# Performance work log

Hardware: AMD Instinct MI355X
Metric: run time of the kernel (lower is better)

Reference implementation:

```python
import jax, jax.numpy as jnp
import numpy as np

N_NODES = 100000
N_EDGES = 1600000
IN_FEATS = 256
DIMS = [IN_FEATS, 128, 64, 16, 40]


def setup_inputs() -> dict:
    key = jax.random.key(0)
    ks = jax.random.split(key, 3 + 2 * 4)
    x = jax.random.normal(ks[0], (N_NODES, IN_FEATS), dtype=jnp.float32)
    src = jax.random.randint(ks[1], (N_EDGES,), 0, N_NODES)
    dst = jax.random.randint(ks[2], (N_EDGES,), 0, N_NODES)
    inp = {"x": x, "src": src, "dst": dst}
    for i in range(4):
        fan_in = DIMS[i]
        inp[f"W{i+1}"] = jax.random.normal(ks[3 + 2 * i], (DIMS[i], DIMS[i + 1]), dtype=jnp.float32) / np.sqrt(fan_in)
        inp[f"b{i+1}"] = jnp.zeros((DIMS[i + 1],), dtype=jnp.float32)
    return inp


def reference(x, src, dst, W1, b1, W2, b2, W3, b3, W4, b4):
    n = x.shape[0]
    ones = jnp.ones(src.shape[0], dtype=x.dtype)
    # symmetric GCN normalization (DGL norm='both'); clamp deg>=1 like DGL
    deg_out = jnp.maximum(jax.ops.segment_sum(ones, src, num_segments=n), 1.0)
    deg_in = jnp.maximum(jax.ops.segment_sum(ones, dst, num_segments=n), 1.0)
    norm_src = jax.lax.rsqrt(deg_out)[:, None]  # [N,1]
    norm_dst = jax.lax.rsqrt(deg_in)[:, None]   # [N,1]

    def gconv(h, W, b, act):
        # project first (in_feats >= out_feats for every layer, matching DGL ordering)
        h = (h * norm_src) @ W                                   # [N, d_out]
        h = jax.ops.segment_sum(h[src], dst, num_segments=n)      # SpMM aggregate
        h = h * norm_dst + b
        return jax.nn.relu(h) if act else h

    h = gconv(x, W1, b1, True)
    h = gconv(h, W2, b2, True)
    h = gconv(h, W3, b3, True)
    h = gconv(h, W4, b4, False)
    return h
```

## Files before the change

kernel.cpp:

```cpp
#include <hip/hip_runtime.h>


typedef unsigned short ushort_t;
#define CAP 64

__device__ __forceinline__ void gload_lds16(const float4* g, float4* l) {
    __builtin_amdgcn_global_load_lds(
        (const __attribute__((address_space(1))) void*)g,
        (__attribute__((address_space(3))) void*)l, 16, 0, 0);
}

__device__ __forceinline__ ushort_t f2bf(float f) {
    unsigned u = __float_as_uint(f);
    u += 0x7FFFu + ((u >> 16) & 1u);
    return (ushort_t)(u >> 16);
}
__device__ __forceinline__ unsigned pack2bf(float a, float b) {
    return (unsigned)f2bf(a) | ((unsigned)f2bf(b) << 16);
}
#define BFLO(u) __uint_as_float((u) << 16)
#define BFHI(u) __uint_as_float((u) & 0xffff0000u)

template<int DIN, int DOUT, int RB, int KT, typename EPI>
__device__ __forceinline__ void proj_body(
        const float* __restrict__ in, const float* __restrict__ W,
        int N, int n0, float4* __restrict__ wlds, float4* __restrict__ xlds,
        EPI&& epi) {
    constexpr int CG  = DOUT / 4;
    constexpr int RPP = 256 / CG;
    constexpr int R4  = RB / RPP;
    constexpr int K4T = KT / 4;
    constexpr int NKT = DIN / KT;
    constexpr int XTILE = RB * K4T;
    constexpr int WTILE = KT * CG;
    static_assert(RPP * CG == 256, "full block");
    static_assert((K4T & (K4T - 1)) == 0, "pow2 swizzle");
    static_assert(XTILE % 256 == 0 && WTILE % 256 == 0, "stage granularity");

    const int tid  = threadIdx.x;
    const int wave = tid >> 6;
    const int lane = tid & 63;
    const int rp   = tid / CG;
    const int cg   = tid - rp * CG;

    float4 acc[R4];
#pragma unroll
    for (int r = 0; r < R4; ++r) acc[r] = make_float4(0.f, 0.f, 0.f, 0.f);

    for (int kt = 0; kt < NKT; ++kt) {
        const float4* wsrc = (const float4*)(W + (size_t)kt * KT * DOUT);
#pragma unroll
        for (int j = 0; j < WTILE / 256; ++j) {
            int base = j * 256 + wave * 64;
            gload_lds16(wsrc + base + lane, &wlds[base]);
        }
#pragma unroll
        for (int j = 0; j < XTILE / 256; ++j) {
            int base = j * 256 + wave * 64;
            int fi   = base + lane;
            int row  = fi / K4T;
            int k4   = fi - row * K4T;
            int k4s  = k4 ^ (row & (K4T - 1));
            int grow = n0 + row; if (grow >= N) grow = N - 1;
            const float4* gsrc = (const float4*)(in + (size_t)grow * DIN) + kt * K4T + k4s;
            gload_lds16(gsrc, &xlds[base]);
        }
        __syncthreads();
#pragma unroll 2
        for (int k4 = 0; k4 < K4T; ++k4) {
            float4 w0 = wlds[(k4 * 4 + 0) * CG + cg];
            float4 w1 = wlds[(k4 * 4 + 1) * CG + cg];
            float4 w2 = wlds[(k4 * 4 + 2) * CG + cg];
            float4 w3 = wlds[(k4 * 4 + 3) * CG + cg];
#pragma unroll
            for (int r = 0; r < R4; ++r) {
                int row = rp + r * RPP;
                float4 xv = xlds[row * K4T + (k4 ^ (row & (K4T - 1)))];
                acc[r].x = fmaf(xv.x, w0.x, acc[r].x);
                acc[r].y = fmaf(xv.x, w0.y, acc[r].y);
                acc[r].z = fmaf(xv.x, w0.z, acc[r].z);
                acc[r].w = fmaf(xv.x, w0.w, acc[r].w);
                acc[r].x = fmaf(xv.y, w1.x, acc[r].x);
                acc[r].y = fmaf(xv.y, w1.y, acc[r].y);
                acc[r].z = fmaf(xv.y, w1.z, acc[r].z);
                acc[r].w = fmaf(xv.y, w1.w, acc[r].w);
                acc[r].x = fmaf(xv.z, w2.x, acc[r].x);
                acc[r].y = fmaf(xv.z, w2.y, acc[r].y);
                acc[r].z = fmaf(xv.z, w2.z, acc[r].z);
                acc[r].w = fmaf(xv.z, w2.w, acc[r].w);
                acc[r].x = fmaf(xv.w, w3.x, acc[r].x);
                acc[r].y = fmaf(xv.w, w3.y, acc[r].y);
                acc[r].z = fmaf(xv.w, w3.z, acc[r].z);
                acc[r].w = fmaf(xv.w, w3.w, acc[r].w);
            }
        }
        __syncthreads();
    }
    epi(acc, rp, cg);
}

template<int DIN, int DOUT, int RB, int KT>
__global__ void __launch_bounds__(256) k_comb(
        const float* __restrict__ x, const float* __restrict__ W,
        ushort_t* __restrict__ outbf, int N,
        const int* __restrict__ src, const int* __restrict__ dst,
        int* __restrict__ degO, int* __restrict__ degI,
        int* __restrict__ colp, int E, int PB, int HTH) {
    constexpr int CG  = DOUT / 4;
    constexpr int RPP = 256 / CG;
    constexpr int R4  = RB / RPP;
    constexpr int K4T = KT / 4;
    __shared__ float4 wlds[KT * CG];
    __shared__ float4 xlds[RB * K4T];

    int bid = blockIdx.x, g = bid / 5, r = bid - g * 5;
    if (r == 4) {
        int i = g * 256 + (int)threadIdx.x;
        for (; i < E; i += HTH) {
            int s = src[i];
            int d = dst[i];
            atomicAdd(&degO[s], 1);
            int rk = atomicAdd(&degI[d], 1);
            if (rk < CAP) colp[(size_t)d * CAP + rk] = s;
        }
        return;
    }
    int pidx = g * 4 + r;
    if (pidx >= PB) return;
    int n0 = pidx * RB;
    proj_body<DIN, DOUT, RB, KT>(x, W, N, n0, wlds, xlds,
        [&](float4 (&acc)[R4], int rp, int cg) {
#pragma unroll
            for (int rr = 0; rr < R4; ++rr) {
                int n = n0 + rp + rr * RPP;
                if (n < N) {
                    ushort4 s;
                    s.x = f2bf(acc[rr].x); s.y = f2bf(acc[rr].y);
                    s.z = f2bf(acc[rr].z); s.w = f2bf(acc[rr].w);
                    *(ushort4*)(outbf + (size_t)n * DOUT + cg * 4) = s;
                }
            }
        });
}

__global__ void k_prep(const int* __restrict__ degO, const int* __restrict__ degI,
                       float* __restrict__ nSf, float* __restrict__ nDf, int N) {
    int i = blockIdx.x * 256 + threadIdx.x;
    if (i < N) {
        int a = degO[i]; nSf[i] = rsqrtf((float)(a > 1 ? a : 1));
        int b = degI[i]; nDf[i] = rsqrtf((float)(b > 1 ? b : 1));
    }
}

__global__ void __launch_bounds__(256) k_proj_l2bf(
        const ushort_t* __restrict__ in, const float* __restrict__ nrm,
        const float* __restrict__ W, ushort_t* __restrict__ outbf, int N) {
    __shared__ float4 wlds[32 * 16];
    __shared__ uint4  xlds[64 * 4];
    const int tid = threadIdx.x;
    const int rp = tid >> 4, cg = tid & 15;
    int n0 = blockIdx.x * 64;

    float4 acc[4];
#pragma unroll
    for (int r = 0; r < 4; ++r) acc[r] = make_float4(0.f, 0.f, 0.f, 0.f);

    for (int kt = 0; kt < 4; ++kt) {
        const float4* wsrc = (const float4*)(W + (size_t)kt * 32 * 64);
        gload_lds16(wsrc + tid, &wlds[tid]);
        gload_lds16(wsrc + 256 + tid, &wlds[256 + tid]);
        {
            int row = tid >> 2, c = tid & 3;
            int cs = c ^ (row & 3);
            int grow = n0 + row; if (grow >= N) grow = N - 1;
            const uint4* gsrc = (const uint4*)(in + (size_t)grow * 128) + kt * 4 + cs;
            gload_lds16((const float4*)gsrc, (float4*)&xlds[tid]);
        }
        __syncthreads();
#pragma unroll
        for (int k8 = 0; k8 < 4; ++k8) {
            float4 w[8];
#pragma unroll
            for (int j = 0; j < 8; ++j) w[j] = wlds[(k8 * 8 + j) * 16 + cg];
#pragma unroll
            for (int r = 0; r < 4; ++r) {
                int row = rp + r * 16;
                uint4 xv = xlds[row * 4 + (k8 ^ (row & 3))];
                float xf[8] = { BFLO(xv.x), BFHI(xv.x), BFLO(xv.y), BFHI(xv.y),
                                BFLO(xv.z), BFHI(xv.z), BFLO(xv.w), BFHI(xv.w) };
#pragma unroll
                for (int j = 0; j < 8; ++j) {
                    acc[r].x = fmaf(xf[j], w[j].x, acc[r].x);
                    acc[r].y = fmaf(xf[j], w[j].y, acc[r].y);
                    acc[r].z = fmaf(xf[j], w[j].z, acc[r].z);
                    acc[r].w = fmaf(xf[j], w[j].w, acc[r].w);
                }
            }
        }
        __syncthreads();
    }
#pragma unroll
    for (int r = 0; r < 4; ++r) {
        int n = n0 + rp + r * 16;
        if (n < N) {
            float nm = nrm[n];
            ushort4 s;
            s.x = f2bf(acc[r].x * nm); s.y = f2bf(acc[r].y * nm);
            s.z = f2bf(acc[r].z * nm); s.w = f2bf(acc[r].w * nm);
            *(ushort4*)(outbf + (size_t)n * 64 + cg * 4) = s;
        }
    }
}

__global__ void __launch_bounds__(256) k_gather_l1(
        const int* __restrict__ colp, const int* __restrict__ degI,
        const float* __restrict__ nSf, const float* __restrict__ nDf,
        const ushort_t* __restrict__ projbf, const float* __restrict__ bias,
        ushort_t* __restrict__ outbf, int N) {
    constexpr int DOUT = 128;
    constexpr int CGB = DOUT / 8;
    long t = blockIdx.x * 256L + threadIdx.x;
    if (t >= (long)N * CGB) return;
    int n  = (int)(t / CGB);
    int cb = (int)(t - (long)n * CGB);
    const int* cl = colp + (size_t)n * CAP;
    int dg = degI[n]; if (dg > CAP) dg = CAP;
    float acc[8];
#pragma unroll
    for (int k = 0; k < 8; ++k) acc[k] = 0.f;
    int i = 0;
    for (; i + 4 <= dg; i += 4) {
        int4 ss = *(const int4*)(cl + i);
        uint4 v0 = *(const uint4*)(projbf + (size_t)ss.x * DOUT + cb * 8);
        uint4 v1 = *(const uint4*)(projbf + (size_t)ss.y * DOUT + cb * 8);
        uint4 v2 = *(const uint4*)(projbf + (size_t)ss.z * DOUT + cb * 8);
        uint4 v3 = *(const uint4*)(projbf + (size_t)ss.w * DOUT + cb * 8);
        float n0 = nSf[ss.x], n1 = nSf[ss.y], n2 = nSf[ss.z], n3 = nSf[ss.w];
        acc[0] = fmaf(n0, BFLO(v0.x), fmaf(n1, BFLO(v1.x), fmaf(n2, BFLO(v2.x), fmaf(n3, BFLO(v3.x), acc[0]))));
        acc[1] = fmaf(n0, BFHI(v0.x), fmaf(n1, BFHI(v1.x), fmaf(n2, BFHI(v2.x), fmaf(n3, BFHI(v3.x), acc[1]))));
        acc[2] = fmaf(n0, BFLO(v0.y), fmaf(n1, BFLO(v1.y), fmaf(n2, BFLO(v2.y), fmaf(n3, BFLO(v3.y), acc[2]))));
        acc[3] = fmaf(n0, BFHI(v0.y), fmaf(n1, BFHI(v1.y), fmaf(n2, BFHI(v2.y), fmaf(n3, BFHI(v3.y), acc[3]))));
        acc[4] = fmaf(n0, BFLO(v0.z), fmaf(n1, BFLO(v1.z), fmaf(n2, BFLO(v2.z), fmaf(n3, BFLO(v3.z), acc[4]))));
        acc[5] = fmaf(n0, BFHI(v0.z), fmaf(n1, BFHI(v1.z), fmaf(n2, BFHI(v2.z), fmaf(n3, BFHI(v3.z), acc[5]))));
        acc[6] = fmaf(n0, BFLO(v0.w), fmaf(n1, BFLO(v1.w), fmaf(n2, BFLO(v2.w), fmaf(n3, BFLO(v3.w), acc[6]))));
        acc[7] = fmaf(n0, BFHI(v0.w), fmaf(n1, BFHI(v1.w), fmaf(n2, BFHI(v2.w), fmaf(n3, BFHI(v3.w), acc[7]))));
    }
    for (; i < dg; ++i) {
        int s0 = cl[i];
        uint4 v0 = *(const uint4*)(projbf + (size_t)s0 * DOUT + cb * 8);
        float ns0 = nSf[s0];
        acc[0] = fmaf(ns0, BFLO(v0.x), acc[0]);
        acc[1] = fmaf(ns0, BFHI(v0.x), acc[1]);
        acc[2] = fmaf(ns0, BFLO(v0.y), acc[2]);
        acc[3] = fmaf(ns0, BFHI(v0.y), acc[3]);
        acc[4] = fmaf(ns0, BFLO(v0.z), acc[4]);
        acc[5] = fmaf(ns0, BFHI(v0.z), acc[5]);
        acc[6] = fmaf(ns0, BFLO(v0.w), acc[6]);
        acc[7] = fmaf(ns0, BFHI(v0.w), acc[7]);
    }
    float nm = nDf[n];
    const float* bp = bias + cb * 8;
    float o[8];
#pragma unroll
    for (int k = 0; k < 8; ++k) o[k] = fmaxf(fmaf(acc[k], nm, bp[k]), 0.f);
    uint4 s;
    s.x = pack2bf(o[0], o[1]); s.y = pack2bf(o[2], o[3]);
    s.z = pack2bf(o[4], o[5]); s.w = pack2bf(o[6], o[7]);
    *(uint4*)(outbf + (size_t)n * DOUT + cb * 8) = s;
}

__global__ void __launch_bounds__(256) k_gather_fuse2(
        const int* __restrict__ colp, const int* __restrict__ degI,
        const float* __restrict__ nSf, const float* __restrict__ nDf,
        const ushort_t* __restrict__ p2bf, const float* __restrict__ b2,
        const float* __restrict__ W3, float* __restrict__ P3, int N) {
    constexpr int DOUT = 64;
    __shared__ float w3s[64 * 16];
    ((float4*)w3s)[threadIdx.x] = ((const float4*)W3)[threadIdx.x];
    __syncthreads();

    long t = blockIdx.x * 256L + threadIdx.x;
    int n = (int)(t >> 3);
    bool valid = n < N;
    if (!valid) n = N - 1;
    int cb = (int)(t & 7);
    int lane = threadIdx.x & 63;
    int gb = lane & ~7;

    const int* cl = colp + (size_t)n * CAP;
    int dg = degI[n]; if (dg > CAP) dg = CAP;
    float acc[8];
#pragma unroll
    for (int k = 0; k < 8; ++k) acc[k] = 0.f;
    int i = 0;
    for (; i + 4 <= dg; i += 4) {
        int4 ss = *(const int4*)(cl + i);
        uint4 v0 = *(const uint4*)(p2bf + (size_t)ss.x * DOUT + cb * 8);
        uint4 v1 = *(const uint4*)(p2bf + (size_t)ss.y * DOUT + cb * 8);
        uint4 v2 = *(const uint4*)(p2bf + (size_t)ss.z * DOUT + cb * 8);
        uint4 v3 = *(const uint4*)(p2bf + (size_t)ss.w * DOUT + cb * 8);
        acc[0] += BFLO(v0.x) + BFLO(v1.x) + BFLO(v2.x) + BFLO(v3.x);
        acc[1] += BFHI(v0.x) + BFHI(v1.x) + BFHI(v2.x) + BFHI(v3.x);
        acc[2] += BFLO(v0.y) + BFLO(v1.y) + BFLO(v2.y) + BFLO(v3.y);
        acc[3] += BFHI(v0.y) + BFHI(v1.y) + BFHI(v2.y) + BFHI(v3.y);
        acc[4] += BFLO(v0.z) + BFLO(v1.z) + BFLO(v2.z) + BFLO(v3.z);
        acc[5] += BFHI(v0.z) + BFHI(v1.z) + BFHI(v2.z) + BFHI(v3.z);
        acc[6] += BFLO(v0.w) + BFLO(v1.w) + BFLO(v2.w) + BFLO(v3.w);
        acc[7] += BFHI(v0.w) + BFHI(v1.w) + BFHI(v2.w) + BFHI(v3.w);
    }
    for (; i < dg; ++i) {
        int s0 = cl[i];
        uint4 v0 = *(const uint4*)(p2bf + (size_t)s0 * DOUT + cb * 8);
        acc[0] += BFLO(v0.x); acc[1] += BFHI(v0.x);
        acc[2] += BFLO(v0.y); acc[3] += BFHI(v0.y);
        acc[4] += BFLO(v0.z); acc[5] += BFHI(v0.z);
        acc[6] += BFLO(v0.w); acc[7] += BFHI(v0.w);
    }
    float nm = nDf[n];
    float ns = nSf[n];
    const float* bp = b2 + cb * 8;
    float o[8];
#pragma unroll
    for (int k = 0; k < 8; ++k)
        o[k] = fmaxf(fmaf(acc[k], nm, bp[k]), 0.f) * ns;
    float y0 = 0.f, y1 = 0.f;
#pragma unroll
    for (int k = 0; k < 64; ++k) {
        float v = __shfl(o[k & 7], gb + (k >> 3), 64);
        y0 = fmaf(v, w3s[k * 16 + 2 * cb], y0);
        y1 = fmaf(v, w3s[k * 16 + 2 * cb + 1], y1);
    }
    if (valid) *(float2*)(P3 + (size_t)n * 16 + 2 * cb) = make_float2(y0, y1);
}

__global__ void __launch_bounds__(256) k_gather_l3(
        const int* __restrict__ colp, const int* __restrict__ degI,
        const float* __restrict__ nSf, const float* __restrict__ nDf,
        const float* __restrict__ proj, const float* __restrict__ bias,
        float* __restrict__ out, int N) {
    long t = blockIdx.x * 256L + threadIdx.x;
    if (t >= (long)N * 4) return;
    int n  = (int)(t >> 2);
    int cg = (int)(t & 3);
    const int* cl = colp + (size_t)n * CAP;
    int dg = degI[n]; if (dg > CAP) dg = CAP;
    float4 a0 = make_float4(0.f, 0.f, 0.f, 0.f);
    float4 a1 = make_float4(0.f, 0.f, 0.f, 0.f);
    float4 a2 = make_float4(0.f, 0.f, 0.f, 0.f);
    float4 a3 = make_float4(0.f, 0.f, 0.f, 0.f);
    int i = 0;
    for (; i + 4 <= dg; i += 4) {
        int4 ss = *(const int4*)(cl + i);
        float4 v0 = *(const float4*)(proj + (size_t)ss.x * 16 + cg * 4);
        float4 v1 = *(const float4*)(proj + (size_t)ss.y * 16 + cg * 4);
        float4 v2 = *(const float4*)(proj + (size_t)ss.z * 16 + cg * 4);
        float4 v3 = *(const float4*)(proj + (size_t)ss.w * 16 + cg * 4);
        a0.x += v0.x; a0.y += v0.y; a0.z += v0.z; a0.w += v0.w;
        a1.x += v1.x; a1.y += v1.y; a1.z += v1.z; a1.w += v1.w;
        a2.x += v2.x; a2.y += v2.y; a2.z += v2.z; a2.w += v2.w;
        a3.x += v3.x; a3.y += v3.y; a3.z += v3.z; a3.w += v3.w;
    }
    for (; i < dg; ++i) {
        int s0 = cl[i];
        float4 v0 = *(const float4*)(proj + (size_t)s0 * 16 + cg * 4);
        a0.x += v0.x; a0.y += v0.y; a0.z += v0.z; a0.w += v0.w;
    }
    float4 s = make_float4(a0.x + a1.x + a2.x + a3.x, a0.y + a1.y + a2.y + a3.y,
                           a0.z + a1.z + a2.z + a3.z, a0.w + a1.w + a2.w + a3.w);
    float nm = nDf[n];
    float ns = nSf[n];
    float4 b = *(const float4*)(bias + cg * 4);
    float4 o;
    o.x = fmaxf(fmaf(s.x, nm, b.x), 0.f) * ns;
    o.y = fmaxf(fmaf(s.y, nm, b.y), 0.f) * ns;
    o.z = fmaxf(fmaf(s.z, nm, b.z), 0.f) * ns;
    o.w = fmaxf(fmaf(s.w, nm, b.w), 0.f) * ns;
    *(float4*)(out + (size_t)n * 16 + cg * 4) = o;
}

__global__ void __launch_bounds__(256) k_gather_fuse4(
        const int* __restrict__ colp, const int* __restrict__ degI,
        const float* __restrict__ nDf, const float* __restrict__ t4,
        const float* __restrict__ W4, const float* __restrict__ b4,
        float* __restrict__ out, int N) {
    __shared__ float w4s[16 * 40];
    __shared__ float b4s[40];
    for (int i = threadIdx.x; i < 160; i += 256)
        ((float4*)w4s)[i] = ((const float4*)W4)[i];
    if (threadIdx.x < 40) b4s[threadIdx.x] = b4[threadIdx.x];
    __syncthreads();

    long t = blockIdx.x * 256L + threadIdx.x;
    int n = (int)(t >> 2);
    bool valid = n < N;
    if (!valid) n = N - 1;
    int cg = (int)(t & 3);
    int lane = threadIdx.x & 63;
    int gb = lane & ~3;

    const int* cl = colp + (size_t)n * CAP;
    int dg = degI[n]; if (dg > CAP) dg = CAP;
    float4 a0 = make_float4(0.f, 0.f, 0.f, 0.f);
    float4 a1 = make_float4(0.f, 0.f, 0.f, 0.f);
    int i = 0;
    for (; i + 2 <= dg; i += 2) {
        int2 ss = *(const int2*)(cl + i);
        float4 v0 = *(const float4*)(t4 + (size_t)ss.x * 16 + cg * 4);
        float4 v1 = *(const float4*)(t4 + (size_t)ss.y * 16 + cg * 4);
        a0.x += v0.x; a0.y += v0.y; a0.z += v0.z; a0.w += v0.w;
        a1.x += v1.x; a1.y += v1.y; a1.z += v1.z; a1.w += v1.w;
    }
    if (i < dg) {
        int s0 = cl[i];
        float4 v0 = *(const float4*)(t4 + (size_t)s0 * 16 + cg * 4);
        a0.x += v0.x; a0.y += v0.y; a0.z += v0.z; a0.w += v0.w;
    }
    float av[4] = { a0.x + a1.x, a0.y + a1.y, a0.z + a1.z, a0.w + a1.w };

    float y[10];
#pragma unroll
    for (int jj = 0; jj < 10; ++jj) y[jj] = 0.f;
#pragma unroll
    for (int k = 0; k < 16; ++k) {
        float v = __shfl(av[k & 3], gb + (k >> 2), 64);
        const float* wr = w4s + k * 40 + cg * 10;
#pragma unroll
        for (int jj = 0; jj < 10; ++jj) y[jj] = fmaf(v, wr[jj], y[jj]);
    }
    if (valid) {
        float nm = nDf[n];
        float* dp = out + (size_t)n * 40 + cg * 10;
        const float* bp = b4s + cg * 10;
#pragma unroll
        for (int jj = 0; jj < 10; ++jj) dp[jj] = fmaf(y[jj], nm, bp[jj]);
    }
}

static inline int cdiv(long a, int b) { return (int)((a + b - 1) / b); }

extern "C" void kernel_launch(void* const* d_in, const int* in_sizes, int n_in,
                              void* d_out, int out_size, void* d_ws, size_t ws_size,
                              hipStream_t stream) {
    const float* x   = (const float*)d_in[0];
    const int*   src = (const int*)d_in[1];
    const int*   dst = (const int*)d_in[2];
    const float* W1 = (const float*)d_in[3];  const float* b1 = (const float*)d_in[4];
    const float* W2 = (const float*)d_in[5];  const float* b2 = (const float*)d_in[6];
    const float* W3 = (const float*)d_in[7];  const float* b3 = (const float*)d_in[8];
    const float* W4 = (const float*)d_in[9];  const float* b4 = (const float*)d_in[10];

    const int N = in_sizes[0] / 256;
    const int E = in_sizes[1];

    int* ws_i = (int*)d_ws;
    int* degO   = ws_i;
    int* degI   = ws_i + N;
    int* colp   = ws_i + 2 * (size_t)N;
    float* nSf  = (float*)(ws_i + 2 * (size_t)N + (size_t)N * CAP);
    float* nDf  = nSf + N;
    float* projb = nDf + N;
    float* hbuf  = projb + (size_t)N * 64;
    ushort_t* projbf = (ushort_t*)projb;
    ushort_t* h1bf   = (ushort_t*)hbuf;
    float* P3 = projb + (size_t)N * 32;

    int PB = cdiv(N, 64);
    int G5 = cdiv(PB, 4);
    int HTH = G5 * 256;

    hipMemsetAsync(degO, 0, 2 * (size_t)N * sizeof(int), stream);
    k_comb<256, 128, 64, 32><<<5 * G5, 256, 0, stream>>>(
        x, W1, projbf, N, src, dst, degO, degI, colp, E, PB, HTH);

    k_prep<<<cdiv(N, 256), 256, 0, stream>>>(degO, degI, nSf, nDf, N);

    k_gather_l1<<<cdiv((long)N * 16, 256), 256, 0, stream>>>(
        colp, degI, nSf, nDf, projbf, b1, h1bf, N);

    k_proj_l2bf<<<cdiv(N, 64), 256, 0, stream>>>(h1bf, nSf, W2, projbf, N);
    k_gather_fuse2<<<cdiv((long)N * 8, 256), 256, 0, stream>>>(
        colp, degI, nSf, nDf, projbf, b2, W3, P3, N);

    k_gather_l3<<<cdiv((long)N * 4, 256), 256, 0, stream>>>(
        colp, degI, nSf, nDf, P3, b3, hbuf, N);

    k_gather_fuse4<<<cdiv((long)N * 4, 256), 256, 0, stream>>>(
        colp, degI, nDf, hbuf, W4, b4, (float*)d_out, N);
}
```

Measured before the change: 353.8 us.

## Split CSR fill by destination half to overlap with layer-1 gather

```diff
diff --git a/kernel.cpp b/kernel.cpp
--- a/kernel.cpp
+++ b/kernel.cpp
@@ -17,6 +17,9 @@
 }
 __device__ __forceinline__ unsigned pack2bf(float a, float b) {
     return (unsigned)f2bf(a) | ((unsigned)f2bf(b) << 16);
+}
+__device__ __forceinline__ float nrm_of(int d) {
+    return rsqrtf((float)(d > 1 ? d : 1));
 }
 #define BFLO(u) __uint_as_float((u) << 16)
 #define BFHI(u) __uint_as_float((u) & 0xffff0000u)
@@ -33,9 +36,6 @@
     constexpr int NKT = DIN / KT;
     constexpr int XTILE = RB * K4T;
     constexpr int WTILE = KT * CG;
-    static_assert(RPP * CG == 256, "full block");
-    static_assert((K4T & (K4T - 1)) == 0, "pow2 swizzle");
-    static_assert(XTILE % 256 == 0 && WTILE % 256 == 0, "stage granularity");
 
     const int tid  = threadIdx.x;
     const int wave = tid >> 6;
@@ -99,13 +99,66 @@
     epi(acc, rp, cg);
 }
 
+__device__ __forceinline__ void gather_l1_body(
+        int n, int cb, const int* __restrict__ colp, const int* __restrict__ degO,
+        const int* __restrict__ degI, const ushort_t* __restrict__ projbf,
+        const float* __restrict__ bias, ushort_t* __restrict__ outbf) {
+    constexpr int DOUT = 128;
+    const int* cl = colp + (size_t)n * CAP;
+    int dgi = degI[n];
+    int dg = dgi > CAP ? CAP : dgi;
+    float acc[8];
+#pragma unroll
+    for (int k = 0; k < 8; ++k) acc[k] = 0.f;
+    int i = 0;
+    for (; i + 4 <= dg; i += 4) {
+        int4 ss = *(const int4*)(cl + i);
+        uint4 v0 = *(const uint4*)(projbf + (size_t)ss.x * DOUT + cb * 8);
+        uint4 v1 = *(const uint4*)(projbf + (size_t)ss.y * DOUT + cb * 8);
+        uint4 v2 = *(const uint4*)(projbf + (size_t)ss.z * DOUT + cb * 8);
+        uint4 v3 = *(const uint4*)(projbf + (size_t)ss.w * DOUT + cb * 8);
+        float n0 = nrm_of(degO[ss.x]), n1 = nrm_of(degO[ss.y]);
+        float n2 = nrm_of(degO[ss.z]), n3 = nrm_of(degO[ss.w]);
+        acc[0] = fmaf(n0, BFLO(v0.x), fmaf(n1, BFLO(v1.x), fmaf(n2, BFLO(v2.x), fmaf(n3, BFLO(v3.x), acc[0]))));
+        acc[1] = fmaf(n0, BFHI(v0.x), fmaf(n1, BFHI(v1.x), fmaf(n2, BFHI(v2.x), fmaf(n3, BFHI(v3.x), acc[1]))));
+        acc[2] = fmaf(n0, BFLO(v0.y), fmaf(n1, BFLO(v1.y), fmaf(n2, BFLO(v2.y), fmaf(n3, BFLO(v3.y), acc[2]))));
+        acc[3] = fmaf(n0, BFHI(v0.y), fmaf(n1, BFHI(v1.y), fmaf(n2, BFHI(v2.y), fmaf(n3, BFHI(v3.y), acc[3]))));
+        acc[4] = fmaf(n0, BFLO(v0.z), fmaf(n1, BFLO(v1.z), fmaf(n2, BFLO(v2.z), fmaf(n3, BFLO(v3.z), acc[4]))));
+        acc[5] = fmaf(n0, BFHI(v0.z), fmaf(n1, BFHI(v1.z), fmaf(n2, BFHI(v2.z), fmaf(n3, BFHI(v3.z), acc[5]))));
+        acc[6] = fmaf(n0, BFLO(v0.w), fmaf(n1, BFLO(v1.w), fmaf(n2, BFLO(v2.w), fmaf(n3, BFLO(v3.w), acc[6]))));
+        acc[7] = fmaf(n0, BFHI(v0.w), fmaf(n1, BFHI(v1.w), fmaf(n2, BFHI(v2.w), fmaf(n3, BFHI(v3.w), acc[7]))));
+    }
+    for (; i < dg; ++i) {
+        int s0 = cl[i];
+        uint4 v0 = *(const uint4*)(projbf + (size_t)s0 * DOUT + cb * 8);
+        float ns0 = nrm_of(degO[s0]);
+        acc[0] = fmaf(ns0, BFLO(v0.x), acc[0]);
+        acc[1] = fmaf(ns0, BFHI(v0.x), acc[1]);
+        acc[2] = fmaf(ns0, BFLO(v0.y), acc[2]);
+        acc[3] = fmaf(ns0, BFHI(v0.y), acc[3]);
+        acc[4] = fmaf(ns0, BFLO(v0.z), acc[4]);
+        acc[5] = fmaf(ns0, BFHI(v0.z), acc[5]);
+        acc[6] = fmaf(ns0, BFLO(v0.w), acc[6]);
+        acc[7] = fmaf(ns0, BFHI(v0.w), acc[7]);
+    }
+    float nm = nrm_of(dgi);
+    const float* bp = bias + cb * 8;
+    float o[8];
+#pragma unroll
+    for (int k = 0; k < 8; ++k) o[k] = fmaxf(fmaf(acc[k], nm, bp[k]), 0.f);
+    uint4 s;
+    s.x = pack2bf(o[0], o[1]); s.y = pack2bf(o[2], o[3]);
+    s.z = pack2bf(o[4], o[5]); s.w = pack2bf(o[6], o[7]);
+    *(uint4*)(outbf + (size_t)n * DOUT + cb * 8) = s;
+}
+
 template<int DIN, int DOUT, int RB, int KT>
-__global__ void __launch_bounds__(256) k_comb(
+__global__ void __launch_bounds__(256) k_combA(
         const float* __restrict__ x, const float* __restrict__ W,
         ushort_t* __restrict__ outbf, int N,
         const int* __restrict__ src, const int* __restrict__ dst,
         int* __restrict__ degO, int* __restrict__ degI,
-        int* __restrict__ colp, int E, int PB, int HTH) {
+        int* __restrict__ colp, int E, int PB, int HTH, int NSPLIT) {
     constexpr int CG  = DOUT / 4;
     constexpr int RPP = 256 / CG;
     constexpr int R4  = RB / RPP;
@@ -120,8 +173,10 @@
             int s = src[i];
             int d = dst[i];
             atomicAdd(&degO[s], 1);
-            int rk = atomicAdd(&degI[d], 1);
-            if (rk < CAP) colp[(size_t)d * CAP + rk] = s;
+            if (d < NSPLIT) {
+                int rk = atomicAdd(&degI[d], 1);
+                if (rk < CAP) colp[(size_t)d * CAP + rk] = s;
+            }
         }
         return;
     }
@@ -143,17 +198,45 @@
         });
 }
 
-__global__ void k_prep(const int* __restrict__ degO, const int* __restrict__ degI,
-                       float* __restrict__ nSf, float* __restrict__ nDf, int N) {
-    int i = blockIdx.x * 256 + threadIdx.x;
-    if (i < N) {
-        int a = degO[i]; nSf[i] = rsqrtf((float)(a > 1 ? a : 1));
-        int b = degI[i]; nDf[i] = rsqrtf((float)(b > 1 ? b : 1));
-    }
+__global__ void __launch_bounds__(256) k_combB(
+        const int* __restrict__ src, const int* __restrict__ dst,
+        int* __restrict__ degI, int* __restrict__ colp,
+        const int* __restrict__ degO, const ushort_t* __restrict__ projbf,
+        const float* __restrict__ b1, ushort_t* __restrict__ h1bf,
+        int NSPLIT, int E, int HTH) {
+    int bid = blockIdx.x, g = bid / 5, r = bid - g * 5;
+    if (r == 4) {
+        int i = g * 256 + (int)threadIdx.x;
+        for (; i < E; i += HTH) {
+            int d = dst[i];
+            if (d >= NSPLIT) {
+                int rk = atomicAdd(&degI[d], 1);
+                if (rk < CAP) colp[(size_t)d * CAP + rk] = src[i];
+            }
+        }
+        return;
+    }
+    long t = ((long)(g * 4 + r)) * 256 + threadIdx.x;
+    if (t >= (long)NSPLIT * 16) return;
+    int n  = (int)(t >> 4);
+    int cb = (int)(t & 15);
+    gather_l1_body(n, cb, colp, degO, degI, projbf, b1, h1bf);
+}
+
+__global__ void __launch_bounds__(256) k_gather_l1(
+        const int* __restrict__ colp, const int* __restrict__ degO,
+        const int* __restrict__ degI, const ushort_t* __restrict__ projbf,
+        const float* __restrict__ bias, ushort_t* __restrict__ outbf,
+        int NSPLIT, int N) {
+    long t = blockIdx.x * 256L + threadIdx.x;
+    if (t >= (long)(N - NSPLIT) * 16) return;
+    int n  = NSPLIT + (int)(t >> 4);
+    int cb = (int)(t & 15);
+    gather_l1_body(n, cb, colp, degO, degI, projbf, bias, outbf);
 }
 
 __global__ void __launch_bounds__(256) k_proj_l2bf(
-        const ushort_t* __restrict__ in, const float* __restrict__ nrm,
+        const ushort_t* __restrict__ in, const int* __restrict__ degO,
         const float* __restrict__ W, ushort_t* __restrict__ outbf, int N) {
     __shared__ float4 wlds[32 * 16];
     __shared__ uint4  xlds[64 * 4];
@@ -203,7 +286,7 @@
     for (int r = 0; r < 4; ++r) {
         int n = n0 + rp + r * 16;
         if (n < N) {
-            float nm = nrm[n];
+            float nm = nrm_of(degO[n]);
             ushort4 s;
             s.x = f2bf(acc[r].x * nm); s.y = f2bf(acc[r].y * nm);
             s.z = f2bf(acc[r].z * nm); s.w = f2bf(acc[r].w * nm);
@@ -212,68 +295,11 @@
     }
 }
 
-__global__ void __launch_bounds__(256) k_gather_l1(
-        const int* __restrict__ colp, const int* __restrict__ degI,
-        const float* __restrict__ nSf, const float* __restrict__ nDf,
-        const ushort_t* __restrict__ projbf, const float* __restrict__ bias,
-        ushort_t* __restrict__ outbf, int N) {
-    constexpr int DOUT = 128;
-    constexpr int CGB = DOUT / 8;
-    long t = blockIdx.x * 256L + threadIdx.x;
-    if (t >= (long)N * CGB) return;
-    int n  = (int)(t / CGB);
-    int cb = (int)(t - (long)n * CGB);
-    const int* cl = colp + (size_t)n * CAP;
-    int dg = degI[n]; if (dg > CAP) dg = CAP;
-    float acc[8];
-#pragma unroll
-    for (int k = 0; k < 8; ++k) acc[k] = 0.f;
-    int i = 0;
-    for (; i + 4 <= dg; i += 4) {
-        int4 ss = *(const int4*)(cl + i);
-        uint4 v0 = *(const uint4*)(projbf + (size_t)ss.x * DOUT + cb * 8);
-        uint4 v1 = *(const uint4*)(projbf + (size_t)ss.y * DOUT + cb * 8);
-        uint4 v2 = *(const uint4*)(projbf + (size_t)ss.z * DOUT + cb * 8);
-        uint4 v3 = *(const uint4*)(projbf + (size_t)ss.w * DOUT + cb * 8);
-        float n0 = nSf[ss.x], n1 = nSf[ss.y], n2 = nSf[ss.z], n3 = nSf[ss.w];
-        acc[0] = fmaf(n0, BFLO(v0.x), fmaf(n1, BFLO(v1.x), fmaf(n2, BFLO(v2.x), fmaf(n3, BFLO(v3.x), acc[0]))));
-        acc[1] = fmaf(n0, BFHI(v0.x), fmaf(n1, BFHI(v1.x), fmaf(n2, BFHI(v2.x), fmaf(n3, BFHI(v3.x), acc[1]))));
-        acc[2] = fmaf(n0, BFLO(v0.y), fmaf(n1, BFLO(v1.y), fmaf(n2, BFLO(v2.y), fmaf(n3, BFLO(v3.y), acc[2]))));
-        acc[3] = fmaf(n0, BFHI(v0.y), fmaf(n1, BFHI(v1.y), fmaf(n2, BFHI(v2.y), fmaf(n3, BFHI(v3.y), acc[3]))));
-        acc[4] = fmaf(n0, BFLO(v0.z), fmaf(n1, BFLO(v1.z), fmaf(n2, BFLO(v2.z), fmaf(n3, BFLO(v3.z), acc[4]))));
-        acc[5] = fmaf(n0, BFHI(v0.z), fmaf(n1, BFHI(v1.z), fmaf(n2, BFHI(v2.z), fmaf(n3, BFHI(v3.z), acc[5]))));
-        acc[6] = fmaf(n0, BFLO(v0.w), fmaf(n1, BFLO(v1.w), fmaf(n2, BFLO(v2.w), fmaf(n3, BFLO(v3.w), acc[6]))));
-        acc[7] = fmaf(n0, BFHI(v0.w), fmaf(n1, BFHI(v1.w), fmaf(n2, BFHI(v2.w), fmaf(n3, BFHI(v3.w), acc[7]))));
-    }
-    for (; i < dg; ++i) {
-        int s0 = cl[i];
-        uint4 v0 = *(const uint4*)(projbf + (size_t)s0 * DOUT + cb * 8);
-        float ns0 = nSf[s0];
-        acc[0] = fmaf(ns0, BFLO(v0.x), acc[0]);
-        acc[1] = fmaf(ns0, BFHI(v0.x), acc[1]);
-        acc[2] = fmaf(ns0, BFLO(v0.y), acc[2]);
-        acc[3] = fmaf(ns0, BFHI(v0.y), acc[3]);
-        acc[4] = fmaf(ns0, BFLO(v0.z), acc[4]);
-        acc[5] = fmaf(ns0, BFHI(v0.z), acc[5]);
-        acc[6] = fmaf(ns0, BFLO(v0.w), acc[6]);
-        acc[7] = fmaf(ns0, BFHI(v0.w), acc[7]);
-    }
-    float nm = nDf[n];
-    const float* bp = bias + cb * 8;
-    float o[8];
-#pragma unroll
-    for (int k = 0; k < 8; ++k) o[k] = fmaxf(fmaf(acc[k], nm, bp[k]), 0.f);
-    uint4 s;
-    s.x = pack2bf(o[0], o[1]); s.y = pack2bf(o[2], o[3]);
-    s.z = pack2bf(o[4], o[5]); s.w = pack2bf(o[6], o[7]);
-    *(uint4*)(outbf + (size_t)n * DOUT + cb * 8) = s;
-}
-
 __global__ void __launch_bounds__(256) k_gather_fuse2(
-        const int* __restrict__ colp, const int* __restrict__ degI,
-        const float* __restrict__ nSf, const float* __restrict__ nDf,
-        const ushort_t* __restrict__ p2bf, const float* __restrict__ b2,
-        const float* __restrict__ W3, float* __restrict__ P3, int N) {
+        const int* __restrict__ colp, const int* __restrict__ degO,
+        const int* __restrict__ degI, const ushort_t* __restrict__ p2bf,
+        const float* __restrict__ b2, const float* __restrict__ W3,
+        float* __restrict__ P3, int N) {
     constexpr int DOUT = 64;
     __shared__ float w3s[64 * 16];
     ((float4*)w3s)[threadIdx.x] = ((const float4*)W3)[threadIdx.x];
@@ -288,7 +314,8 @@
     int gb = lane & ~7;
 
     const int* cl = colp + (size_t)n * CAP;
-    int dg = degI[n]; if (dg > CAP) dg = CAP;
+    int dgi = degI[n];
+    int dg = dgi > CAP ? CAP : dgi;
     float acc[8];
 #pragma unroll
     for (int k = 0; k < 8; ++k) acc[k] = 0.f;
@@ -316,8 +343,8 @@
         acc[4] += BFLO(v0.z); acc[5] += BFHI(v0.z);
         acc[6] += BFLO(v0.w); acc[7] += BFHI(v0.w);
     }
-    float nm = nDf[n];
-    float ns = nSf[n];
+    float nm = nrm_of(dgi);
+    float ns = nrm_of(degO[n]);
     const float* bp = b2 + cb * 8;
     float o[8];
 #pragma unroll
@@ -334,16 +361,16 @@
 }
 
 __global__ void __launch_bounds__(256) k_gather_l3(
-        const int* __restrict__ colp, const int* __restrict__ degI,
-        const float* __restrict__ nSf, const float* __restrict__ nDf,
-        const float* __restrict__ proj, const float* __restrict__ bias,
-        float* __restrict__ out, int N) {
+        const int* __restrict__ colp, const int* __restrict__ degO,
+        const int* __restrict__ degI, const float* __restrict__ proj,
+        const float* __restrict__ bias, float* __restrict__ out, int N) {
     long t = blockIdx.x * 256L + threadIdx.x;
     if (t >= (long)N * 4) return;
     int n  = (int)(t >> 2);
     int cg = (int)(t & 3);
     const int* cl = colp + (size_t)n * CAP;
-    int dg = degI[n]; if (dg > CAP) dg = CAP;
+    int dgi = degI[n];
+    int dg = dgi > CAP ? CAP : dgi;
     float4 a0 = make_float4(0.f, 0.f, 0.f, 0.f);
     float4 a1 = make_float4(0.f, 0.f, 0.f, 0.f);
     float4 a2 = make_float4(0.f, 0.f, 0.f, 0.f);
@@ -367,8 +394,8 @@
     }
     float4 s = make_float4(a0.x + a1.x + a2.x + a3.x, a0.y + a1.y + a2.y + a3.y,
                            a0.z + a1.z + a2.z + a3.z, a0.w + a1.w + a2.w + a3.w);
-    float nm = nDf[n];
-    float ns = nSf[n];
+    float nm = nrm_of(dgi);
+    float ns = nrm_of(degO[n]);
     float4 b = *(const float4*)(bias + cg * 4);
     float4 o;
     o.x = fmaxf(fmaf(s.x, nm, b.x), 0.f) * ns;
@@ -380,9 +407,8 @@
 
 __global__ void __launch_bounds__(256) k_gather_fuse4(
         const int* __restrict__ colp, const int* __restrict__ degI,
-        const float* __restrict__ nDf, const float* __restrict__ t4,
-        const float* __restrict__ W4, const float* __restrict__ b4,
-        float* __restrict__ out, int N) {
+        const float* __restrict__ t4, const float* __restrict__ W4,
+        const float* __restrict__ b4, float* __restrict__ out, int N) {
     __shared__ float w4s[16 * 40];
     __shared__ float b4s[40];
     for (int i = threadIdx.x; i < 160; i += 256)
@@ -399,7 +425,8 @@
     int gb = lane & ~3;
 
     const int* cl = colp + (size_t)n * CAP;
-    int dg = degI[n]; if (dg > CAP) dg = CAP;
+    int dgi = degI[n];
+    int dg = dgi > CAP ? CAP : dgi;
     float4 a0 = make_float4(0.f, 0.f, 0.f, 0.f);
     float4 a1 = make_float4(0.f, 0.f, 0.f, 0.f);
     int i = 0;
@@ -428,7 +455,7 @@
         for (int jj = 0; jj < 10; ++jj) y[jj] = fmaf(v, wr[jj], y[jj]);
     }
     if (valid) {
-        float nm = nDf[n];
+        float nm = nrm_of(dgi);
         float* dp = out + (size_t)n * 40 + cg * 10;
         const float* bp = b4s + cg * 10;
 #pragma unroll
@@ -451,39 +478,44 @@
 
     const int N = in_sizes[0] / 256;
     const int E = in_sizes[1];
+    const int NSPLIT = ((N / 2) + 63) / 64 * 64;
 
     int* ws_i = (int*)d_ws;
     int* degO   = ws_i;
     int* degI   = ws_i + N;
     int* colp   = ws_i + 2 * (size_t)N;
-    float* nSf  = (float*)(ws_i + 2 * (size_t)N + (size_t)N * CAP);
-    float* nDf  = nSf + N;
-    float* projb = nDf + N;
+    float* projb = (float*)(ws_i + 2 * (size_t)N + (size_t)N * CAP);
     float* hbuf  = projb + (size_t)N * 64;
     ushort_t* projbf = (ushort_t*)projb;
     ushort_t* h1bf   = (ushort_t*)hbuf;
     float* P3 = projb + (size_t)N * 32;
 
-    int PB = cdiv(N, 64);
-    int G5 = cdiv(PB, 4);
-    int HTH = G5 * 256;
+    int PB  = cdiv(N, 64);
+    int G5A = cdiv(PB, 4);
+    int HTHA = G5A * 256;
+
+    long tA = (long)NSPLIT * 16;
+    int GBB = cdiv(tA, 256);
+    int G5B = cdiv(GBB, 4);
+    int HTHB = G5B * 256;
 
     hipMemsetAsync(degO, 0, 2 * (size_t)N * sizeof(int), stream);
-    k_comb<256, 128, 64, 32><<<5 * G5, 256, 0, stream>>>(
-        x, W1, projbf, N, src, dst, degO, degI, colp, E, PB, HTH);
-
-    k_prep<<<cdiv(N, 256), 256, 0, stream>>>(degO, degI, nSf, nDf, N);
-
-    k_gather_l1<<<cdiv((long)N * 16, 256), 256, 0, stream>>>(
-        colp, degI, nSf, nDf, projbf, b1, h1bf, N);
-
-    k_proj_l2bf<<<cdiv(N, 64), 256, 0, stream>>>(h1bf, nSf, W2, projbf, N);
+    k_combA<256, 128, 64, 32><<<5 * G5A, 256, 0, stream>>>(
+        x, W1, projbf, N, src, dst, degO, degI, colp, E, PB, HTHA, NSPLIT);
+
+    k_combB<<<5 * G5B, 256, 0, stream>>>(
+        src, dst, degI, colp, degO, projbf, b1, h1bf, NSPLIT, E, HTHB);
+
+    k_gather_l1<<<cdiv((long)(N - NSPLIT) * 16, 256), 256, 0, stream>>>(
+        colp, degO, degI, projbf, b1, h1bf, NSPLIT, N);
+
+    k_proj_l2bf<<<cdiv(N, 64), 256, 0, stream>>>(h1bf, degO, W2, projbf, N);
     k_gather_fuse2<<<cdiv((long)N * 8, 256), 256, 0, stream>>>(
-        colp, degI, nSf, nDf, projbf, b2, W3, P3, N);
+        colp, degO, degI, projbf, b2, W3, P3, N);
 
     k_gather_l3<<<cdiv((long)N * 4, 256), 256, 0, stream>>>(
-        colp, degI, nSf, nDf, P3, b3, hbuf, N);
+        colp, degO, degI, P3, b3, hbuf, N);
 
     k_gather_fuse4<<<cdiv((long)N * 4, 256), 256, 0, stream>>>(
-        colp, degI, nDf, hbuf, W4, b4, (float*)d_out, N);
-}
+        colp, degI, hbuf, W4, b4, (float*)d_out, N);
+}
```

Measured after the change: 343.4 us. 1.03x faster.
